# Performance work log

Hardware: AMD Instinct MI355X
Metric: run time of the kernel (lower is better)

The kernel has to match this reference:

```python
import jax, jax.numpy as jnp
import numpy as np

IN, HID, BATCH = 1024, 1024, 4096


def _linear_params(key, out_dim, in_dim):
    # torch.nn.Linear default init: U(-1/sqrt(in), 1/sqrt(in))
    k1, k2 = jax.random.split(key)
    bound = 1.0 / np.sqrt(in_dim)
    w = jax.random.uniform(k1, (out_dim, in_dim), jnp.float32, -bound, bound)
    b = jax.random.uniform(k2, (out_dim,), jnp.float32, -bound, bound)
    return w, b


def setup_inputs() -> dict:
    key = jax.random.key(0)
    keys = jax.random.split(key, 11)
    inp = {
        'input': jax.random.normal(keys[0], (BATCH, IN), jnp.float32),
        'h': jax.random.normal(keys[1], (BATCH, HID), jnp.float32),
        'c': jax.random.normal(keys[2], (BATCH, HID), jnp.float32),
    }
    names = ['i_i', 'i_h', 'f_i', 'f_h', 'g_i', 'g_h', 'o_i', 'o_h']
    for n, k in zip(names, keys[3:]):
        in_dim = IN if n.endswith('_i') else HID
        w, b = _linear_params(k, HID, in_dim)
        inp['w_' + n] = w
        inp['b_' + n] = b
    return inp


def reference(input, h, c,
              w_i_i, b_i_i, w_i_h, b_i_h,
              w_f_i, b_f_i, w_f_h, b_f_h,
              w_g_i, b_g_i, w_g_h, b_g_h,
              w_o_i, b_o_i, w_o_h, b_o_h):
    def lin(x, w, b):
        return x @ w.T + b

    i = jax.nn.sigmoid(lin(input, w_i_i, b_i_i) + lin(h, w_i_h, b_i_h))
    f = jax.nn.sigmoid(lin(input, w_f_i, b_f_i) + lin(h, w_f_h, b_f_h))
    g = jnp.tanh(lin(input, w_g_i, b_g_i) + lin(h, w_g_h, b_g_h))
    o = jax.nn.sigmoid(lin(input, w_o_i, b_o_i) + lin(h, w_o_h, b_o_h))
    c_prime = f * c + i * g
    h_prime = o * jnp.tanh(c_prime)
    return (h_prime, c_prime)
```

## Files before the change

kernel.cpp:

```cpp
#include <hip/hip_runtime.h>
#include <stdint.h>

#define BATCH 4096
#define IN_DIM 1024
#define HID 1024
#define KDIM 2048
#define NGATE 4096
#define EPITCH 136
#define BK 64
#define BM 256
#define BN 128

typedef __attribute__((ext_vector_type(4))) float floatx4;
typedef __attribute__((ext_vector_type(8))) __bf16 bf16x8;
typedef __attribute__((ext_vector_type(8))) unsigned short ushort8;

__device__ __forceinline__ unsigned short f2bf(float f) {
    union { float f; unsigned int u; } v; v.f = f;
    unsigned int u = v.u;
    u += 0x7fffu + ((u >> 16) & 1u);
    return (unsigned short)(u >> 16);
}
__device__ __forceinline__ float bf2f(unsigned short s) {
    union { unsigned int u; float f; } v; v.u = ((unsigned int)s) << 16;
    return v.f;
}
__device__ __forceinline__ ushort8 cvt8(const float* __restrict__ src) {
    float4 v0 = ((const float4*)src)[0];
    float4 v1 = ((const float4*)src)[1];
    ushort8 o = { f2bf(v0.x), f2bf(v0.y), f2bf(v0.z), f2bf(v0.w),
                  f2bf(v1.x), f2bf(v1.y), f2bf(v1.z), f2bf(v1.w) };
    return o;
}

__global__ __launch_bounds__(256) void prep_kernel(
    const float* __restrict__ x,  const float* __restrict__ h,
    const float* __restrict__ wii, const float* __restrict__ wih,
    const float* __restrict__ wfi, const float* __restrict__ wfh,
    const float* __restrict__ wgi, const float* __restrict__ wgh,
    const float* __restrict__ woi, const float* __restrict__ woh,
    const float* __restrict__ bii, const float* __restrict__ bih,
    const float* __restrict__ bfi, const float* __restrict__ bfh,
    const float* __restrict__ bgi, const float* __restrict__ bgh,
    const float* __restrict__ boi, const float* __restrict__ boh,
    unsigned short* __restrict__ Xb,
    unsigned short* __restrict__ Wb,
    float* __restrict__ bias)
{
    const int bid = blockIdx.x;
    const int tid = threadIdx.x;

    if (bid < 2048) {
        const int e = (bid * 256 + tid) * 8;
        const int b = e >> 10, k = e & 1023;
        *(ushort8*)(Xb + (size_t)b * KDIM + k) = cvt8(x + e);
    } else if (bid < 4096) {
        const int e = ((bid - 2048) * 256 + tid) * 8;
        const int b = e >> 10, k = e & 1023;
        *(ushort8*)(Xb + (size_t)b * KDIM + 1024 + k) = cvt8(h + e);
    } else if (bid < 8192) {
        const int m   = (bid - 4096) >> 9;
        const int off = (bid - 4096) & 511;
        const int e = (off * 256 + tid) * 8;
        const int n = e >> 10, k = e & 1023;
        const float* src;
        switch (m) {
            case 0: src = wii; break; case 1: src = wih; break;
            case 2: src = wfi; break; case 3: src = wfh; break;
            case 4: src = wgi; break; case 5: src = wgh; break;
            case 6: src = woi; break; default: src = woh; break;
        }
        const int gate = m >> 1, part = m & 1;
        *(ushort8*)(Wb + (size_t)(n * 4 + gate) * KDIM + part * 1024 + k)
            = cvt8(src + e);
    } else {
        const int t = (bid - 8192) * 256 + tid;
        const int gate = (bid - 8192) >> 2;
        const int n = t & 1023;
        const float *bi, *bh_;
        switch (gate) {
            case 0: bi = bii; bh_ = bih; break;
            case 1: bi = bfi; bh_ = bfh; break;
            case 2: bi = bgi; bh_ = bgh; break;
            default: bi = boi; bh_ = boh; break;
        }
        bias[n * 4 + gate] = bi[n] + bh_[n];
    }
}

#define GLD16(g, l)                                                          \
    __builtin_amdgcn_global_load_lds(                                        \
        (__attribute__((address_space(1))) void*)(g),                        \
        (__attribute__((address_space(3))) void*)(l), 16, 0, 0)

__global__ __launch_bounds__(512) void gemm_lstm(
    const unsigned short* __restrict__ X,
    const unsigned short* __restrict__ W,
    const float* __restrict__ bias,
    const float* __restrict__ c_in,
    float* __restrict__ out)
{
    __shared__ __align__(16) unsigned char smem[49152];
    unsigned short* As = (unsigned short*)smem;
    unsigned short* Bs = (unsigned short*)(smem + 32768);
    unsigned short* E  = (unsigned short*)smem;

    const int tid  = threadIdx.x;
    const int wave = tid >> 6;
    const int lane = tid & 63;
    const int quad = lane >> 4, idx = lane & 15;
    const int wm = (wave >> 1) * 64;
    const int wn = (wave & 1) * 64;

    const int l   = blockIdx.x;
    const int xcd = l & 7;
    const int s   = l >> 3;
    const int bx  = xcd * 2 + (s >> 5);
    const int by  = s & 31;
    const int rowA0 = bx * BM;
    const int rowB0 = by * BN;

    const int srow = tid >> 3;
    const int skk  = ((tid & 7) ^ (srow & 7)) * 8;
    const unsigned short* gA = X + (size_t)(rowA0 + srow) * KDIM + skk;
    const unsigned short* gB = W + (size_t)(rowB0 + srow) * KDIM + skk;
    const size_t rstride = (size_t)64 * KDIM;

    const int swz = (idx & 7);

    floatx4 acc[4][4] = {};

    for (int k0 = 0; k0 < KDIM; k0 += BK) {
#pragma unroll
        for (int r = 0; r < 4; ++r)
            GLD16(gA + k0 + r * rstride, As + (r * 512 + tid) * 8);
#pragma unroll
        for (int r = 0; r < 2; ++r)
            GLD16(gB + k0 + r * rstride, Bs + (r * 512 + tid) * 8);
        __syncthreads();

        bf16x8 af[4][2], bfr[4][2];
#pragma unroll
        for (int t = 0; t < 2; ++t) {
            const int co = ((t * 4 + quad) ^ swz) * 8;
#pragma unroll
            for (int i = 0; i < 4; ++i)
                af[i][t] = *(const bf16x8*)(As + (wm + i * 16 + idx) * BK + co);
#pragma unroll
            for (int j = 0; j < 4; ++j)
                bfr[j][t] = *(const bf16x8*)(Bs + (wn + j * 16 + idx) * BK + co);
        }
#pragma unroll
        for (int t = 0; t < 2; ++t)
#pragma unroll
            for (int i = 0; i < 4; ++i)
#pragma unroll
                for (int j = 0; j < 4; ++j)
                    acc[i][j] = __builtin_amdgcn_mfma_f32_16x16x32_bf16(
                        af[i][t], bfr[j][t], acc[i][j], 0, 0, 0);
        __syncthreads();
    }

    const int g = idx & 3;
    const int tid8 = tid & 7;
    const int rowo = tid >> 3;
    float* __restrict__ out_h = out;
    float* __restrict__ out_c = out + (size_t)BATCH * HID;

#pragma unroll
    for (int half = 0; half < 2; ++half) {
        if ((wave >> 2) == half) {
            const int wml = wm - half * 128;
#pragma unroll
            for (int j = 0; j < 4; ++j) {
                const int col = wn + j * 16 + idx;
                const float bv = bias[rowB0 + col];
#pragma unroll
                for (int i = 0; i < 4; ++i) {
#pragma unroll
                    for (int r = 0; r < 4; ++r) {
                        const int row = wml + i * 16 + quad * 4 + r;
                        const float v  = acc[i][j][r] + bv;
                        const float vv = (g == 2) ? 2.f * v : v;
                        const float s2 = 1.f / (1.f + __expf(-vv));
                        const float a  = (g == 2) ? 2.f * s2 - 1.f : s2;
                        E[row * EPITCH + col] = f2bf(a);
                    }
                }
            }
        }
        __syncthreads();

#pragma unroll
        for (int p = 0; p < 2; ++p) {
            const int row_l = p * 64 + rowo;
            const int row_g = rowA0 + half * 128 + row_l;
            const int colc  = tid8 * 16;
            ushort8 e0 = *(const ushort8*)(E + row_l * EPITCH + colc);
            ushort8 e1 = *(const ushort8*)(E + row_l * EPITCH + colc + 8);
            const int u0 = (rowB0 >> 2) + tid8 * 4;
            const float4 cv = *(const float4*)(c_in + (size_t)row_g * HID + u0);

            float cvv[4] = { cv.x, cv.y, cv.z, cv.w };
            float hp[4], cp[4];
#pragma unroll
            for (int d = 0; d < 4; ++d) {
                const ushort8& e = (d < 2) ? e0 : e1;
                const int b = (d & 1) * 4;
                const float iv = bf2f(e[b + 0]);
                const float fv = bf2f(e[b + 1]);
                const float gv = bf2f(e[b + 2]);
                const float ov = bf2f(e[b + 3]);
                const float c2 = fv * cvv[d] + iv * gv;
                const float e2 = __expf(2.f * c2);
                cp[d] = c2;
                hp[d] = ov * ((e2 - 1.f) / (e2 + 1.f));
            }
            float4 hv  = { hp[0], hp[1], hp[2], hp[3] };
            float4 cpv = { cp[0], cp[1], cp[2], cp[3] };
            *(float4*)(out_h + (size_t)row_g * HID + u0) = hv;
            *(float4*)(out_c + (size_t)row_g * HID + u0) = cpv;
        }
        __syncthreads();
    }
}

extern "C" void kernel_launch(void* const* d_in, const int* in_sizes, int n_in,
                              void* d_out, int out_size, void* d_ws, size_t ws_size,
                              hipStream_t stream) {
    const float* x   = (const float*)d_in[0];
    const float* h   = (const float*)d_in[1];
    const float* c   = (const float*)d_in[2];
    const float* wii = (const float*)d_in[3];
    const float* bii = (const float*)d_in[4];
    const float* wih = (const float*)d_in[5];
    const float* bih = (const float*)d_in[6];
    const float* wfi = (const float*)d_in[7];
    const float* bfi = (const float*)d_in[8];
    const float* wfh = (const float*)d_in[9];
    const float* bfh = (const float*)d_in[10];
    const float* wgi = (const float*)d_in[11];
    const float* bgi = (const float*)d_in[12];
    const float* wgh = (const float*)d_in[13];
    const float* bgh = (const float*)d_in[14];
    const float* woi = (const float*)d_in[15];
    const float* boi = (const float*)d_in[16];
    const float* woh = (const float*)d_in[17];
    const float* boh = (const float*)d_in[18];

    char* ws = (char*)d_ws;
    unsigned short* Xb  = (unsigned short*)ws;
    unsigned short* Wb  = (unsigned short*)(ws + ((size_t)16 << 20));
    float*          bsv = (float*)(ws + ((size_t)32 << 20));

    prep_kernel<<<8208, 256, 0, stream>>>(
        x, h, wii, wih, wfi, wfh, wgi, wgh, woi, woh,
        bii, bih, bfi, bfh, bgi, bgh, boi, boh, Xb, Wb, bsv);

    gemm_lstm<<<(BATCH / BM) * (NGATE / BN), 512, 0, stream>>>(
        Xb, Wb, bsv, c, (float*)d_out);
}
```

Before: 214.6 us.

## Double-buffer LDS tiles with BK=32 to overlap global loads with MFMA

Halves the K tile to 32 and splits shared memory into two buffers, so the async global-to-LDS load for the next K step is issued before computing on the current one. This drops one barrier per iteration and hides load latency behind the MFMAs. The swizzle pattern is adapted to the narrower 4-chunk rows. In exchange there are twice as many iterations, each with less MFMA work per barrier, and the swizzle may leave more LDS bank conflicts.

Result: slower. 220.8 us (+2.9%).

```diff
diff --git a/kernel.cpp b/kernel.cpp
--- a/kernel.cpp
+++ b/kernel.cpp
@@ -7,7 +7,7 @@
 #define KDIM 2048
 #define NGATE 4096
 #define EPITCH 136
-#define BK 64
+#define BK 32
 #define BM 256
 #define BN 128
 
@@ -101,8 +101,6 @@
     float* __restrict__ out)
 {
     __shared__ __align__(16) unsigned char smem[49152];
-    unsigned short* As = (unsigned short*)smem;
-    unsigned short* Bs = (unsigned short*)(smem + 32768);
     unsigned short* E  = (unsigned short*)smem;
 
     const int tid  = threadIdx.x;
@@ -120,46 +118,54 @@
     const int rowA0 = bx * BM;
     const int rowB0 = by * BN;
 
-    const int srow = tid >> 3;
-    const int skk  = ((tid & 7) ^ (srow & 7)) * 8;
+    const int srow = tid >> 2;
+    const int skk  = ((tid & 3) ^ ((tid >> 3) & 3)) * 8;
     const unsigned short* gA = X + (size_t)(rowA0 + srow) * KDIM + skk;
     const unsigned short* gB = W + (size_t)(rowB0 + srow) * KDIM + skk;
-    const size_t rstride = (size_t)64 * KDIM;
-
-    const int swz = (idx & 7);
+    const size_t rstride = (size_t)128 * KDIM;
+
+    const int co = ((quad ^ ((idx >> 1) & 3)) & 3) * 8;
 
     floatx4 acc[4][4] = {};
 
-    for (int k0 = 0; k0 < KDIM; k0 += BK) {
-#pragma unroll
-        for (int r = 0; r < 4; ++r)
-            GLD16(gA + k0 + r * rstride, As + (r * 512 + tid) * 8);
-#pragma unroll
-        for (int r = 0; r < 2; ++r)
-            GLD16(gB + k0 + r * rstride, Bs + (r * 512 + tid) * 8);
+    {
+        unsigned short* As = (unsigned short*)(smem);
+        unsigned short* Bs = (unsigned short*)(smem + 16384);
+        GLD16(gA,            As + tid * 8);
+        GLD16(gA + rstride,  As + (512 + tid) * 8);
+        GLD16(gB,            Bs + tid * 8);
+    }
+
+    const int NIT = KDIM / BK;
+    for (int it = 0; it < NIT; ++it) {
         __syncthreads();
 
-        bf16x8 af[4][2], bfr[4][2];
-#pragma unroll
-        for (int t = 0; t < 2; ++t) {
-            const int co = ((t * 4 + quad) ^ swz) * 8;
-#pragma unroll
-            for (int i = 0; i < 4; ++i)
-                af[i][t] = *(const bf16x8*)(As + (wm + i * 16 + idx) * BK + co);
+        if (it + 1 < NIT) {
+            unsigned short* As = (unsigned short*)(smem + ((it + 1) & 1) * 24576);
+            unsigned short* Bs = As + 8192;
+            const int k0 = (it + 1) * BK;
+            GLD16(gA + k0,            As + tid * 8);
+            GLD16(gA + k0 + rstride,  As + (512 + tid) * 8);
+            GLD16(gB + k0,            Bs + tid * 8);
+        }
+
+        const unsigned short* As = (const unsigned short*)(smem + (it & 1) * 24576);
+        const unsigned short* Bs = As + 8192;
+        bf16x8 af[4], bfr[4];
+#pragma unroll
+        for (int i = 0; i < 4; ++i)
+            af[i] = *(const bf16x8*)(As + (wm + i * 16 + idx) * BK + co);
+#pragma unroll
+        for (int j = 0; j < 4; ++j)
+            bfr[j] = *(const bf16x8*)(Bs + (wn + j * 16 + idx) * BK + co);
+#pragma unroll
+        for (int i = 0; i < 4; ++i)
 #pragma unroll
             for (int j = 0; j < 4; ++j)
-                bfr[j][t] = *(const bf16x8*)(Bs + (wn + j * 16 + idx) * BK + co);
-        }
-#pragma unroll
-        for (int t = 0; t < 2; ++t)
-#pragma unroll
-            for (int i = 0; i < 4; ++i)
-#pragma unroll
-                for (int j = 0; j < 4; ++j)
-                    acc[i][j] = __builtin_amdgcn_mfma_f32_16x16x32_bf16(
-                        af[i][t], bfr[j][t], acc[i][j], 0, 0, 0);
-        __syncthreads();
-    }
+                acc[i][j] = __builtin_amdgcn_mfma_f32_16x16x32_bf16(
+                    af[i], bfr[j], acc[i][j], 0, 0, 0);
+    }
+    __syncthreads();
 
     const int g = idx & 3;
     const int tid8 = tid & 7;
```
